# Kernel tuning notes

Hardware: AMD Instinct MI355X
Metric: run time of the kernel (lower is better)

Reference implementation:

```python
import jax, jax.numpy as jnp
import numpy as np

B, N, F, I = 4, 1024, 32, 8
DIM, DN, NF = 256, 64, 100
H, HD = 4, 64  # heads, head_dim (H*HD == DIM)
EPS = 1e-5


def setup_inputs() -> dict:
    key = jax.random.key(0)
    ks = jax.random.split(key, 24)
    def p(k, shape, s=0.05):
        return jax.random.normal(k, shape, jnp.float32) * s
    return {
        "x": jax.random.normal(ks[0], (B, N, F, I), jnp.float32),
        "idx": jax.random.randint(ks[1], (F,), 0, NF),
        "ctx": jax.random.normal(ks[2], (B, 1, DN), jnp.float32),
        "Wp": p(ks[3], (NF, DIM * I)),          # in_projection table
        "Bp": p(ks[4], (NF, DIM)),               # feature_bias table
        "q_emb": p(ks[5], (1, DIM)),             # queries table
        "cln_kv_W": p(ks[6], (DN, 2 * DIM)), "cln_kv_b": jnp.zeros((2 * DIM,), jnp.float32),
        "cln_q_W": p(ks[7], (DN, 2 * DIM)),  "cln_q_b": jnp.zeros((2 * DIM,), jnp.float32),
        "cln_h_W": p(ks[8], (DN, 2 * DIM)),  "cln_h_b": jnp.zeros((2 * DIM,), jnp.float32),
        "Wq": p(ks[9], (DIM, DIM)), "Wk": p(ks[10], (DIM, DIM)),
        "Wv": p(ks[11], (DIM, DIM)), "Wo": p(ks[12], (DIM, DIM)),
        "W1": p(ks[13], (DIM, 4 * DIM)), "b1": jnp.zeros((4 * DIM,), jnp.float32),
        "W2": p(ks[14], (4 * DIM, DIM)), "b2": jnp.zeros((DIM,), jnp.float32),
    }


def _ln(x):
    m = x.mean(-1, keepdims=True)
    v = ((x - m) ** 2).mean(-1, keepdims=True)
    return (x - m) * jax.lax.rsqrt(v + EPS)


def _cln(x, c, W, b):
    # adaptive layernorm: ln(x) * (1 + scale(ctx)) + shift(ctx)
    h = _ln(x)
    s, sh = jnp.split(c @ W + b, 2, axis=-1)
    return h * (1.0 + s) + sh


def reference(x, idx, ctx, Wp, Bp, q_emb, cln_kv_W, cln_kv_b, cln_q_W, cln_q_b,
              cln_h_W, cln_h_b, Wq, Wk, Wv, Wo, W1, b1, W2, b2):
    b_, n_, f_, i_ = x.shape
    # gather per-feature projection weights and biases
    w = Wp[idx].reshape(f_, DIM, i_)                 # [f, d, i]
    bias = Bp[idx][None]                              # [1, f, d] (broadcasts b,n)
    kv = jnp.einsum('bnfi,fdi->bnfd', x, w)           # [b, n, f, d]
    c = ctx[:, :, None, :]                            # [b, 1, 1, dn]
    kv = _cln(kv, c, cln_kv_W, cln_kv_b) + bias
    q = jnp.broadcast_to(q_emb[None, None], (b_, n_, 1, DIM))
    # cross-attention (pre-norm, conditional)
    qn = _cln(q, c, cln_q_W, cln_q_b)
    qh = (qn @ Wq).reshape(b_, n_, 1, H, HD)
    kh = (kv @ Wk).reshape(b_, n_, f_, H, HD)
    vh = (kv @ Wv).reshape(b_, n_, f_, H, HD)
    att = jnp.einsum('bnqhe,bnfhe->bnhqf', qh, kh) / np.sqrt(HD).astype(np.float32)
    att = jax.nn.softmax(att, axis=-1)
    o = jnp.einsum('bnhqf,bnfhe->bnqhe', att, vh).reshape(b_, n_, 1, DIM) @ Wo
    h = q + o
    # MLP (pre-norm, conditional)
    hn = _cln(h, c, cln_h_W, cln_h_b)
    h = h + (jax.nn.gelu(hn @ W1 + b1) @ W2 + b2)
    return h[:, :, 0, :]                              # squeeze query dim -> [b, n, d]
```

## Files before the change

kernel.cpp:

```cpp
#include <hip/hip_runtime.h>
#include <cmath>

#define EPSV 1e-5f
using f4 = float4;

typedef __attribute__((ext_vector_type(8))) short bfrag;
typedef __attribute__((ext_vector_type(4))) float ffrag;

#define WS_SKV   0
#define WS_SHKV  1024
#define WS_SH    2048
#define WS_SHH   3072
#define WS_A     4096
#define WS_R     8192
#define WS_HT    4202496
#define WS_L     5251072
#define WS_G     6299648
#define WS_GB    WS_G
#define WS_HNB   (WS_G + 2097152)
#define WS_W1T   (WS_G + 2621440)
#define WS_W2T   (WS_G + 2752512)
#define WS_MT    (WS_G + 2883584)

#define FMA8(acc, s, wa, wb) \
  acc[0]=fmaf((s),(wa).x,acc[0]); acc[1]=fmaf((s),(wa).y,acc[1]); \
  acc[2]=fmaf((s),(wa).z,acc[2]); acc[3]=fmaf((s),(wa).w,acc[3]); \
  acc[4]=fmaf((s),(wb).x,acc[4]); acc[5]=fmaf((s),(wb).y,acc[5]); \
  acc[6]=fmaf((s),(wb).z,acc[6]); acc[7]=fmaf((s),(wb).w,acc[7]);

#define DOT8(res, v, wa, wb) \
  res = fmaf((v)[0],(wa).x,res); res = fmaf((v)[1],(wa).y,res); \
  res = fmaf((v)[2],(wa).z,res); res = fmaf((v)[3],(wa).w,res); \
  res = fmaf((v)[4],(wb).x,res); res = fmaf((v)[5],(wb).y,res); \
  res = fmaf((v)[6],(wb).z,res); res = fmaf((v)[7],(wb).w,res);

__device__ __forceinline__ float bfly32(float v){
  v += __shfl_xor(v, 1);  v += __shfl_xor(v, 2);  v += __shfl_xor(v, 4);
  v += __shfl_xor(v, 8);  v += __shfl_xor(v, 16);
  return v;
}

__device__ __forceinline__ float gelu_fast(float x){
  float z2 = 1.5957691216057308f*(x + 0.044715f*x*x*x);
  return x / (1.0f + __expf(-z2));
}

__device__ __forceinline__ unsigned short f2bf(float x){
  union { float f; unsigned u; } v; v.f = x;
  unsigned r = v.u + 0x7fffu + ((v.u >> 16) & 1u);
  return (unsigned short)(r >> 16);
}
__device__ __forceinline__ void bf2x(unsigned u, float& a, float& b){
  union { unsigned u; float f; } x, y;
  x.u = u << 16; y.u = u & 0xffff0000u;
  a = x.f; b = y.f;
}

__global__ __launch_bounds__(256) void kw_conv(
  const float* __restrict__ W1, const float* __restrict__ W2,
  float* __restrict__ ws)
{
  __shared__ unsigned short lt[64][68];
  const int tid = threadIdx.x;
  int blk = blockIdx.x;
  const float* src; unsigned short* dst; int K, N, K0, N0;
  if (blk < 64){
    src = W1; dst = (unsigned short*)(ws + WS_W1T);
    K = 256; N = 1024; K0 = (blk >> 4)*64; N0 = (blk & 15)*64;
  } else {
    blk -= 64;
    src = W2; dst = (unsigned short*)(ws + WS_W2T);
    K = 1024; N = 256; K0 = (blk >> 2)*64; N0 = (blk & 3)*64;
  }
  #pragma unroll
  for (int i=0;i<4;++i){
    int r = i*16 + (tid>>4);
    int c = (tid&15)*4;
    f4 v = *(const f4*)(src + (size_t)(K0+r)*N + N0 + c);
    lt[r][c]   = f2bf(v.x); lt[r][c+1] = f2bf(v.y);
    lt[r][c+2] = f2bf(v.z); lt[r][c+3] = f2bf(v.w);
  }
  __syncthreads();
  #pragma unroll
  for (int i=0;i<4;++i){
    int n  = i*16 + (tid>>4);
    int kc = (tid&15)*4;
    ushort4 u;
    u.x = lt[kc][n]; u.y = lt[kc+1][n]; u.z = lt[kc+2][n]; u.w = lt[kc+3][n];
    *(ushort4*)(dst + (size_t)(N0+n)*K + K0 + kc) = u;
  }
}

__global__ __launch_bounds__(256) void km_conv(
  const float* __restrict__ Wv, const float* __restrict__ Wo,
  float* __restrict__ ws)
{
  __shared__ float wvs[4*64];
  __shared__ float wos[64*256];
  const int tid = threadIdx.x;
  const int h   = blockIdx.x >> 6;
  const int dg4 = blockIdx.x & 63;
  {
    int d = tid >> 6, e = tid & 63;
    wvs[d*64+e] = Wv[(size_t)(dg4*4 + d)*256 + h*64 + e];
  }
  {
    int e = tid >> 2, c = (tid & 3)*64;
    const float* src = Wo + (size_t)(h*64 + e)*256 + c;
    #pragma unroll
    for (int i=0;i<16;++i)
      *(f4*)&wos[e*256 + c + i*4] = *(const f4*)(src + i*4);
  }
  __syncthreads();
  float acc[4] = {};
  for (int e=0;e<64;++e){
    float wo = wos[e*256 + tid];
    acc[0] = fmaf(wvs[0*64+e], wo, acc[0]);
    acc[1] = fmaf(wvs[1*64+e], wo, acc[1]);
    acc[2] = fmaf(wvs[2*64+e], wo, acc[2]);
    acc[3] = fmaf(wvs[3*64+e], wo, acc[3]);
  }
  unsigned short* Mt = (unsigned short*)(ws + WS_MT);
  ushort4 u;
  u.x = f2bf(acc[0]); u.y = f2bf(acc[1]); u.z = f2bf(acc[2]); u.w = f2bf(acc[3]);
  *(ushort4*)(Mt + (size_t)tid*1024 + h*256 + dg4*4) = u;
}

__global__ __launch_bounds__(256) void k0_all(
    const float* __restrict__ ctx, const float* __restrict__ q_emb,
    const float* __restrict__ Wkv, const float* __restrict__ bkv,
    const float* __restrict__ Wqc, const float* __restrict__ bqc,
    const float* __restrict__ Whc, const float* __restrict__ bhc,
    const float* __restrict__ Wq,  const float* __restrict__ Wk,
    float* __restrict__ ws)
{
  const int b = blockIdx.x >> 2, h = blockIdx.x & 3;
  const int tid = threadIdx.x;
  __shared__ float c[64], qn[256], ph[256], qh64[64], red[8];
  if (tid < 64) c[tid] = ctx[b*64 + tid];
  __syncthreads();

  float skv = bkv[tid],      shkv = bkv[256+tid];
  float sq  = bqc[tid],      shq  = bqc[256+tid];
  float sh  = bhc[tid],      shh  = bhc[256+tid];
  #pragma unroll 8
  for (int j=0;j<64;++j){
    float cj = c[j];
    skv  = fmaf(cj, Wkv[j*512 + tid],       skv);
    shkv = fmaf(cj, Wkv[j*512 + 256 + tid], shkv);
    sq   = fmaf(cj, Wqc[j*512 + tid],       sq);
    shq  = fmaf(cj, Wqc[j*512 + 256 + tid], shq);
    sh   = fmaf(cj, Whc[j*512 + tid],       sh);
    shh  = fmaf(cj, Whc[j*512 + 256 + tid], shh);
  }
  if (h == 0){
    ws[WS_SKV  + b*256 + tid] = skv;
    ws[WS_SHKV + b*256 + tid] = shkv;
    ws[WS_SH   + b*256 + tid] = sh;
    ws[WS_SHH  + b*256 + tid] = shh;
  }

  float qe = q_emb[tid];
  float s1r = qe, s2r = qe*qe;
  for (int mm=1;mm<64;mm<<=1){ s1r += __shfl_xor(s1r,mm); s2r += __shfl_xor(s2r,mm); }
  int wv = tid>>6, ln = tid&63;
  if (ln==0){ red[wv*2]=s1r; red[wv*2+1]=s2r; }
  __syncthreads();
  float S1 = red[0]+red[2]+red[4]+red[6];
  float S2 = red[1]+red[3]+red[5]+red[7];
  float mean = S1*(1.0f/256.0f);
  float var  = S2*(1.0f/256.0f) - mean*mean;
  float rs   = rsqrtf(var + EPSV);
  qn[tid] = (qe-mean)*rs*(1.0f+sq) + shq;
  __syncthreads();

  {
    const int t = tid & 63, ks = tid >> 6;
    float p = 0.f;
    const float* wq = Wq + (size_t)(ks*64)*256 + h*64 + t;
    #pragma unroll 8
    for (int d=0; d<64; ++d) p = fmaf(qn[ks*64+d], wq[d*256], p);
    ph[tid] = p;
  }
  __syncthreads();
  if (tid < 64) qh64[tid] = ph[tid] + ph[64+tid] + ph[128+tid] + ph[192+tid];
  __syncthreads();

  {
    float a = 0.f;
    const float* wkr = Wk + (size_t)tid*256 + h*64;
    #pragma unroll
    for (int e4=0; e4<16; ++e4){
      f4 wv4 = *(const f4*)(wkr + e4*4);
      a = fmaf(qh64[e4*4+0], wv4.x, a);
      a = fmaf(qh64[e4*4+1], wv4.y, a);
      a = fmaf(qh64[e4*4+2], wv4.z, a);
      a = fmaf(qh64[e4*4+3], wv4.w, a);
    }
    ws[WS_A + b*1024 + h*256 + tid] = 0.125f*a;
  }
}

__global__ __launch_bounds__(256,4) void k1f_attn(
  const float* __restrict__ x, const int* __restrict__ idx,
  const float* __restrict__ Wp, const float* __restrict__ Bp,
  float* __restrict__ ws)
{
  __shared__ float xs[2048];
  __shared__ float wls[4096];
  __shared__ float As[1024];

  const int tid = threadIdx.x;
  const int p0  = (blockIdx.x >> 1) * 8;
  const int half= blockIdx.x & 1;
  const int f0  = half * 16;
  const int b   = p0 >> 10;
  const int t   = tid >> 5;
  const int dg  = tid & 31;
  const int dA  = 4*dg, dB = 128 + 4*dg;

  {
    const float* xg = x + (size_t)p0*256 + tid*8;
    f4 a  = *(const f4*)xg;
    f4 bq = *(const f4*)(xg + 4);
    *(f4*)&xs[tid*8]     = a;
    *(f4*)&xs[tid*8 + 4] = bq;
  }
  *(f4*)&As[tid*4] = *(const f4*)(ws + WS_A + b*1024 + tid*4);

  f4 skA = *(const f4*)(ws + WS_SKV  + b*256 + dA);
  f4 skB = *(const f4*)(ws + WS_SKV  + b*256 + dB);
  f4 shA = *(const f4*)(ws + WS_SHKV + b*256 + dA);
  f4 shB = *(const f4*)(ws + WS_SHKV + b*256 + dB);
  float coef[8] = {1.f+skA.x,1.f+skA.y,1.f+skA.z,1.f+skA.w,
                   1.f+skB.x,1.f+skB.y,1.f+skB.z,1.f+skB.w};
  float shk[8]  = {shA.x,shA.y,shA.z,shA.w, shB.x,shB.y,shB.z,shB.w};

  int r0 = idx[f0], r1 = idx[f0+1];
  f4 u0 = *(const f4*)(Wp + (size_t)r0*2048 + tid*8);
  f4 u1 = *(const f4*)(Wp + (size_t)r0*2048 + tid*8 + 4);
  f4 u2 = *(const f4*)(Wp + (size_t)r1*2048 + tid*8);
  f4 u3 = *(const f4*)(Wp + (size_t)r1*2048 + tid*8 + 4);

  float l[4] = {0.f,0.f,0.f,0.f};
  float racc[4][8] = {};

  for (int fi = 0; fi < 8; ++fi){
    const int f = f0 + fi*2;
    __syncthreads();
    wls[0*256+tid]=u0.x; wls[1*256+tid]=u0.y; wls[2*256+tid]=u0.z; wls[3*256+tid]=u0.w;
    wls[4*256+tid]=u1.x; wls[5*256+tid]=u1.y; wls[6*256+tid]=u1.z; wls[7*256+tid]=u1.w;
    wls[2048+0*256+tid]=u2.x; wls[2048+1*256+tid]=u2.y;
    wls[2048+2*256+tid]=u2.z; wls[2048+3*256+tid]=u2.w;
    wls[2048+4*256+tid]=u3.x; wls[2048+5*256+tid]=u3.y;
    wls[2048+6*256+tid]=u3.z; wls[2048+7*256+tid]=u3.w;
    __syncthreads();

    f4 ba0 = *(const f4*)(Bp + (size_t)r0*256 + dA);
    f4 bb0 = *(const f4*)(Bp + (size_t)r0*256 + dB);
    f4 ba1 = *(const f4*)(Bp + (size_t)r1*256 + dA);
    f4 bb1 = *(const f4*)(Bp + (size_t)r1*256 + dB);

    const int fn = (fi < 7) ? f + 2 : f0;
    int rn0 = idx[fn], rn1 = idx[fn+1];
    u0 = *(const f4*)(Wp + (size_t)rn0*2048 + tid*8);
    u1 = *(const f4*)(Wp + (size_t)rn0*2048 + tid*8 + 4);
    u2 = *(const f4*)(Wp + (size_t)rn1*2048 + tid*8);
    u3 = *(const f4*)(Wp + (size_t)rn1*2048 + tid*8 + 4);

    #pragma unroll
    for (int sub=0; sub<2; ++sub){
      const float* wrow = wls + sub*2048;
      const int fc = f + sub;
      f4 ba = sub ? ba1 : ba0;
      f4 bb = sub ? bb1 : bb0;

      f4 xa = *(const f4*)&xs[t*256 + fc*8];
      f4 xb = *(const f4*)&xs[t*256 + fc*8 + 4];
      float xf[8] = {xa.x,xa.y,xa.z,xa.w, xb.x,xb.y,xb.z,xb.w};

      float val[8] = {};
      #pragma unroll
      for (int i=0;i<8;++i){
        f4 wa  = *(const f4*)&wrow[i*256 + dA];
        f4 wbv = *(const f4*)&wrow[i*256 + dB];
        FMA8(val, xf[i], wa, wbv);
      }

      float s=0.f, ss=0.f;
      #pragma unroll
      for (int jj=0;jj<8;++jj){ s += val[jj]; ss = fmaf(val[jj],val[jj],ss); }
      s = bfly32(s); ss = bfly32(ss);
      float mean = s*(1.f/256.f);
      float var  = ss*(1.f/256.f) - mean*mean;
      float rsg  = rsqrtf(var + EPSV);
      float mrs  = mean*rsg;

      float off[8] = {shk[0]+ba.x, shk[1]+ba.y, shk[2]+ba.z, shk[3]+ba.w,
                      shk[4]+bb.x, shk[5]+bb.y, shk[6]+bb.z, shk[7]+bb.w};
      float kvl[8];
      #pragma unroll
      for (int jj=0;jj<8;++jj)
        kvl[jj] = fmaf(fmaf(val[jj], rsg, -mrs), coef[jj], off[jj]);

      #pragma unroll
      for (int h=0;h<4;++h){
        f4 Aa = *(const f4*)&As[h*256 + dA];
        f4 Ab = *(const f4*)&As[h*256 + dB];
        float lg = 0.f;
        DOT8(lg, kvl, Aa, Ab);
        lg = bfly32(lg);
        float pp = __expf(lg);
        l[h] += pp;
        #pragma unroll
        for (int jj=0;jj<8;++jj)
          racc[h][jj] = fmaf(pp, kvl[jj], racc[h][jj]);
      }
    }
    r0 = rn0; r1 = rn1;
  }

  unsigned short* Pr = (unsigned short*)(ws + WS_R);
  size_t base = (size_t)(half*4096 + p0 + t) * 1024;
  #pragma unroll
  for (int h=0;h<4;++h){
    ushort4 ua, ub;
    ua.x=f2bf(racc[h][0]); ua.y=f2bf(racc[h][1]); ua.z=f2bf(racc[h][2]); ua.w=f2bf(racc[h][3]);
    ub.x=f2bf(racc[h][4]); ub.y=f2bf(racc[h][5]); ub.z=f2bf(racc[h][6]); ub.w=f2bf(racc[h][7]);
    *(ushort4*)(Pr + base + h*256 + dA) = ua;
    *(ushort4*)(Pr + base + h*256 + dB) = ub;
  }
  if (dg == 0){
    float* Lp = ws + WS_L;
    #pragma unroll
    for (int h=0;h<4;++h) Lp[(size_t)(half*4096 + p0 + t)*4 + h] = l[h];
  }
}

__global__ __launch_bounds__(256) void kc_comb(float* __restrict__ ws)
{
  unsigned short* Pr = (unsigned short*)(ws + WS_R);
  const float* Lp = ws + WS_L;
  const int tid = threadIdx.x;
  const int p0 = blockIdx.x * 8;
  #pragma unroll
  for (int k=0;k<4;++k){
    size_t e0 = (size_t)p0*1024 + (size_t)k*2048 + (size_t)tid*8;
    int t = (int)(e0 >> 10);
    int h = (int)((e0 >> 8) & 3);
    float inv = 1.f / (Lp[(size_t)t*4 + h] + Lp[(size_t)(4096 + t)*4 + h]);
    uint4 a  = *(const uint4*)(Pr + e0);
    uint4 bq = *(const uint4*)(Pr + 4194304 + e0);
    unsigned au[4] = {a.x, a.y, a.z, a.w};
    unsigned bu[4] = {bq.x, bq.y, bq.z, bq.w};
    unsigned r[4];
    #pragma unroll
    for (int i=0;i<4;++i){
      float alo, ahi, blo, bhi;
      bf2x(au[i], alo, ahi);
      bf2x(bu[i], blo, bhi);
      float lo = (alo + blo) * inv;
      float hi = (ahi + bhi) * inv;
      r[i] = ((unsigned)f2bf(hi) << 16) | (unsigned)f2bf(lo);
    }
    *(uint4*)(Pr + e0) = make_uint4(r[0], r[1], r[2], r[3]);
  }
}

__global__ __launch_bounds__(256) void k2g_mfma(float* __restrict__ ws)
{
  __shared__ unsigned short aT[2][32*40];
  __shared__ unsigned short bT[2][64*40];
  const unsigned short* rb = (const unsigned short*)(ws + WS_R);
  const unsigned short* mt = (const unsigned short*)(ws + WS_MT);

  const int tid = threadIdx.x;
  const int M0 = (blockIdx.x >> 2) * 32;
  const int N0 = (blockIdx.x & 3) * 64;
  const int lane = tid & 63;
  const int wid = tid >> 6;
  const int wm = wid >> 1, wn = wid & 1;
  const int m16 = lane & 15, q = lane >> 4;

  const int sa_m = tid >> 3, sa_k = (tid & 7) * 4;
  const int sb_n = tid >> 2, sb_k = (tid & 3) * 8;

  ushort4 ua;
  f4 ub;
  ua = *(const ushort4*)(rb + (size_t)(M0 + sa_m)*1024 + sa_k);
  ub = *(const f4*)(mt + (size_t)(N0 + sb_n)*1024 + sb_k);

  ffrag acc[2];
  acc[0] = (ffrag){0.f,0.f,0.f,0.f};
  acc[1] = (ffrag){0.f,0.f,0.f,0.f};

  for (int ks=0; ks<32; ++ks){
    const int buf = ks & 1;
    *(ushort4*)&aT[buf][sa_m*40 + sa_k] = ua;
    *(f4*)&bT[buf][sb_n*40 + sb_k]      = ub;
    __syncthreads();
    int kn = (ks < 31) ? ks+1 : 31;
    ua = *(const ushort4*)(rb + (size_t)(M0 + sa_m)*1024 + kn*32 + sa_k);
    ub = *(const f4*)(mt + (size_t)(N0 + sb_n)*1024 + kn*32 + sb_k);

    bfrag af, bf0, bf1;
    af  = *(const bfrag*)&aT[buf][(wm*16 + m16)*40 + q*8];
    bf0 = *(const bfrag*)&bT[buf][(wn*32 + m16)*40 + q*8];
    bf1 = *(const bfrag*)&bT[buf][(wn*32 + 16 + m16)*40 + q*8];
    acc[0] = __builtin_amdgcn_mfma_f32_16x16x32_bf16(bf0, af, acc[0], 0, 0, 0);
    acc[1] = __builtin_amdgcn_mfma_f32_16x16x32_bf16(bf1, af, acc[1], 0, 0, 0);
  }

  const int m = M0 + wm*16 + m16;
  #pragma unroll
  for (int j=0;j<2;++j){
    const int n4 = N0 + wn*32 + j*16 + q*4;
    *(f4*)(ws + WS_HT + (size_t)m*256 + n4) =
      make_float4(acc[j][0], acc[j][1], acc[j][2], acc[j][3]);
  }
}

__global__ __launch_bounds__(256) void ke_ln(
  const float* __restrict__ q_emb, float* __restrict__ ws)
{
  const int tid = threadIdx.x;
  const int p0 = blockIdx.x * 8;
  const int b  = p0 >> 10;
  const int tq = tid >> 5, jq = tid & 31;
  const int cA = 4*jq, cB = 128 + 4*jq;

  float* op = ws + WS_HT + (size_t)(p0+tq)*256;
  f4 oA = *(const f4*)(op + cA);
  f4 oB = *(const f4*)(op + cB);
  f4 qA = *(const f4*)(q_emb + cA);
  f4 qB = *(const f4*)(q_emb + cB);
  float ht[8] = {oA.x+qA.x, oA.y+qA.y, oA.z+qA.z, oA.w+qA.w,
                 oB.x+qB.x, oB.y+qB.y, oB.z+qB.z, oB.w+qB.w};
  float s=0.f, ss=0.f;
  #pragma unroll
  for (int jj=0;jj<8;++jj){ s += ht[jj]; ss = fmaf(ht[jj],ht[jj],ss); }
  s = bfly32(s); ss = bfly32(ss);
  float mean = s*(1.f/256.f);
  float var  = ss*(1.f/256.f) - mean*mean;
  float rsg  = rsqrtf(var + EPSV);
  f4 sH0 = *(const f4*)(ws + WS_SH  + b*256 + cA);
  f4 sH1 = *(const f4*)(ws + WS_SH  + b*256 + cB);
  f4 hH0 = *(const f4*)(ws + WS_SHH + b*256 + cA);
  f4 hH1 = *(const f4*)(ws + WS_SHH + b*256 + cB);
  float sHv[8]  = {sH0.x,sH0.y,sH0.z,sH0.w, sH1.x,sH1.y,sH1.z,sH1.w};
  float hHv[8]  = {hH0.x,hH0.y,hH0.z,hH0.w, hH1.x,hH1.y,hH1.z,hH1.w};
  float hnv[8];
  #pragma unroll
  for (int jj=0;jj<8;++jj)
    hnv[jj] = (ht[jj]-mean)*rsg*(1.f+sHv[jj]) + hHv[jj];

  *(f4*)(op+cA) = make_float4(ht[0],ht[1],ht[2],ht[3]);
  *(f4*)(op+cB) = make_float4(ht[4],ht[5],ht[6],ht[7]);
  unsigned short* hnb = (unsigned short*)(ws + WS_HNB);
  ushort4 uA, uB;
  uA.x=f2bf(hnv[0]); uA.y=f2bf(hnv[1]); uA.z=f2bf(hnv[2]); uA.w=f2bf(hnv[3]);
  uB.x=f2bf(hnv[4]); uB.y=f2bf(hnv[5]); uB.z=f2bf(hnv[6]); uB.w=f2bf(hnv[7]);
  *(ushort4*)(hnb + (size_t)(p0+tq)*256 + cA) = uA;
  *(ushort4*)(hnb + (size_t)(p0+tq)*256 + cB) = uB;
}

__global__ __launch_bounds__(256) void k3_mfma(
  const float* __restrict__ b1, float* __restrict__ ws)
{
  __shared__ unsigned short aT[2][64*40];
  __shared__ unsigned short bT[2][128*40];
  const unsigned short* hnb = (const unsigned short*)(ws + WS_HNB);
  const unsigned short* w1t = (const unsigned short*)(ws + WS_W1T);
  unsigned short* gb = (unsigned short*)(ws + WS_GB);

  const int tid = threadIdx.x;
  const int M0 = (blockIdx.x >> 3) * 64;
  const int N0 = (blockIdx.x & 7) * 128;
  const int lane = tid & 63;
  const int wid = tid >> 6;
  const int wm = wid >> 1, wn = wid & 1;
  const int m16 = lane & 15, q = lane >> 4;

  const int sa_m = tid >> 2, sa_k = (tid & 3) * 8;
  const int sb_n = tid >> 1, sb_k = (tid & 1) * 16;

  f4 ua, ub0, ub1;
  ua  = *(const f4*)(hnb + (size_t)(M0 + sa_m)*256 + sa_k);
  ub0 = *(const f4*)(w1t + (size_t)(N0 + sb_n)*256 + sb_k);
  ub1 = *(const f4*)(w1t + (size_t)(N0 + sb_n)*256 + sb_k + 8);

  ffrag acc[2][4];
  #pragma unroll
  for (int i=0;i<2;++i)
    #pragma unroll
    for (int j=0;j<4;++j) acc[i][j] = (ffrag){0.f,0.f,0.f,0.f};

  for (int ks=0; ks<8; ++ks){
    const int buf = ks & 1;
    *(f4*)&aT[buf][sa_m*40 + sa_k]     = ua;
    *(f4*)&bT[buf][sb_n*40 + sb_k]     = ub0;
    *(f4*)&bT[buf][sb_n*40 + sb_k + 8] = ub1;
    __syncthreads();
    int kn = (ks < 7) ? ks+1 : 7;
    ua  = *(const f4*)(hnb + (size_t)(M0 + sa_m)*256 + kn*32 + sa_k);
    ub0 = *(const f4*)(w1t + (size_t)(N0 + sb_n)*256 + kn*32 + sb_k);
    ub1 = *(const f4*)(w1t + (size_t)(N0 + sb_n)*256 + kn*32 + sb_k + 8);

    bfrag af[2], bf_[4];
    af[0] = *(const bfrag*)&aT[buf][(wm*32 + m16)*40 + q*8];
    af[1] = *(const bfrag*)&aT[buf][(wm*32 + 16 + m16)*40 + q*8];
    #pragma unroll
    for (int j=0;j<4;++j)
      bf_[j] = *(const bfrag*)&bT[buf][(wn*64 + j*16 + m16)*40 + q*8];
    #pragma unroll
    for (int i=0;i<2;++i)
      #pragma unroll
      for (int j=0;j<4;++j)
        acc[i][j] = __builtin_amdgcn_mfma_f32_16x16x32_bf16(bf_[j], af[i], acc[i][j], 0, 0, 0);
  }

  #pragma unroll
  for (int i=0;i<2;++i){
    const int m = M0 + wm*32 + i*16 + m16;
    #pragma unroll
    for (int j=0;j<4;++j){
      const int n4 = N0 + wn*64 + j*16 + q*4;
      f4 bv = *(const f4*)(b1 + n4);
      ushort4 u;
      u.x = f2bf(gelu_fast(acc[i][j][0] + bv.x));
      u.y = f2bf(gelu_fast(acc[i][j][1] + bv.y));
      u.z = f2bf(gelu_fast(acc[i][j][2] + bv.z));
      u.w = f2bf(gelu_fast(acc[i][j][3] + bv.w));
      *(ushort4*)(gb + (size_t)m*1024 + n4) = u;
    }
  }
}

__global__ __launch_bounds__(256) void k4_mfma(
  const float* __restrict__ b2, const float* __restrict__ ws_c,
  float* __restrict__ ws, float* __restrict__ out)
{
  __shared__ unsigned short aT[2][32*40];
  __shared__ unsigned short bT[2][64*40];
  const unsigned short* gb  = (const unsigned short*)(ws_c + WS_GB);
  const unsigned short* w2t = (const unsigned short*)(ws_c + WS_W2T);

  const int tid = threadIdx.x;
  const int M0 = (blockIdx.x >> 2) * 32;
  const int N0 = (blockIdx.x & 3) * 64;
  const int lane = tid & 63;
  const int wid = tid >> 6;
  const int wm = wid >> 1, wn = wid & 1;
  const int m16 = lane & 15, q = lane >> 4;

  const int sa_m = tid >> 3, sa_k = (tid & 7) * 4;
  const int sb_n = tid >> 2, sb_k = (tid & 3) * 8;

  ushort4 ua;
  f4 ub;
  ua = *(const ushort4*)(gb  + (size_t)(M0 + sa_m)*1024 + sa_k);
  ub = *(const f4*)(w2t + (size_t)(N0 + sb_n)*1024 + sb_k);

  ffrag acc[2];
  acc[0] = (ffrag){0.f,0.f,0.f,0.f};
  acc[1] = (ffrag){0.f,0.f,0.f,0.f};

  for (int ks=0; ks<32; ++ks){
    const int buf = ks & 1;
    *(ushort4*)&aT[buf][sa_m*40 + sa_k] = ua;
    *(f4*)&bT[buf][sb_n*40 + sb_k]      = ub;
    __syncthreads();
    int kn = (ks < 31) ? ks+1 : 31;
    ua = *(const ushort4*)(gb  + (size_t)(M0 + sa_m)*1024 + kn*32 + sa_k);
    ub = *(const f4*)(w2t + (size_t)(N0 + sb_n)*1024 + kn*32 + sb_k);

    bfrag af, bf0, bf1;
    af  = *(const bfrag*)&aT[buf][(wm*16 + m16)*40 + q*8];
    bf0 = *(const bfrag*)&bT[buf][(wn*32 + m16)*40 + q*8];
    bf1 = *(const bfrag*)&bT[buf][(wn*32 + 16 + m16)*40 + q*8];
    acc[0] = __builtin_amdgcn_mfma_f32_16x16x32_bf16(bf0, af, acc[0], 0, 0, 0);
    acc[1] = __builtin_amdgcn_mfma_f32_16x16x32_bf16(bf1, af, acc[1], 0, 0, 0);
  }

  const int m = M0 + wm*16 + m16;
  #pragma unroll
  for (int j=0;j<2;++j){
    const int n4 = N0 + wn*32 + j*16 + q*4;
    f4 bv = *(const f4*)(b2 + n4);
    f4 hv = *(const f4*)(ws + WS_HT + (size_t)m*256 + n4);
    *(f4*)(out + (size_t)m*256 + n4) =
      make_float4(acc[j][0]+bv.x+hv.x, acc[j][1]+bv.y+hv.y,
                  acc[j][2]+bv.z+hv.z, acc[j][3]+bv.w+hv.w);
  }
}

extern "C" void kernel_launch(void* const* d_in, const int* in_sizes, int n_in,
                              void* d_out, int out_size, void* d_ws, size_t ws_size,
                              hipStream_t stream)
{
  const float* x    = (const float*)d_in[0];
  const int*   idx  = (const int*)  d_in[1];
  const float* ctx  = (const float*)d_in[2];
  const float* Wp   = (const float*)d_in[3];
  const float* Bp   = (const float*)d_in[4];
  const float* qemb = (const float*)d_in[5];
  const float* Wkv  = (const float*)d_in[6];
  const float* bkv  = (const float*)d_in[7];
  const float* Wqc  = (const float*)d_in[8];
  const float* bqc  = (const float*)d_in[9];
  const float* Whc  = (const float*)d_in[10];
  const float* bhc  = (const float*)d_in[11];
  const float* Wq   = (const float*)d_in[12];
  const float* Wk   = (const float*)d_in[13];
  const float* Wv   = (const float*)d_in[14];
  const float* Wo   = (const float*)d_in[15];
  const float* W1   = (const float*)d_in[16];
  const float* b1   = (const float*)d_in[17];
  const float* W2   = (const float*)d_in[18];
  const float* b2   = (const float*)d_in[19];
  float* ws  = (float*)d_ws;
  float* out = (float*)d_out;

  hipLaunchKernelGGL(kw_conv,  dim3(128),  dim3(256), 0, stream, W1, W2, ws);
  hipLaunchKernelGGL(km_conv,  dim3(256),  dim3(256), 0, stream, Wv, Wo, ws);
  hipLaunchKernelGGL(k0_all,   dim3(16),   dim3(256), 0, stream,
                     ctx, qemb, Wkv, bkv, Wqc, bqc, Whc, bhc, Wq, Wk, ws);
  hipLaunchKernelGGL(k1f_attn, dim3(1024), dim3(256), 0, stream, x, idx, Wp, Bp, ws);
  hipLaunchKernelGGL(kc_comb,  dim3(512),  dim3(256), 0, stream, ws);
  hipLaunchKernelGGL(k2g_mfma, dim3(512),  dim3(256), 0, stream, ws);
  hipLaunchKernelGGL(ke_ln,    dim3(512),  dim3(256), 0, stream, qemb, ws);
  hipLaunchKernelGGL(k3_mfma,  dim3(512),  dim3(256), 0, stream, b1, ws);
  hipLaunchKernelGGL(k4_mfma,  dim3(512),  dim3(256), 0, stream, b2, ws, ws, out);
}
```

Before: 202.7 us.

## Fuse split-softmax combine into GEMM, merge weight-convert kernels, use DPP reductions

The separate kernel that combined the two feature-half partial attention outputs is removed. Its normalization by the summed softmax denominators now happens inside the MFMA GEMM's A-tile staging, which loads both partial buffers and scales them on the fly. This removes one launch and a full read-modify-write pass over the partial outputs. The two weight-conversion kernels are merged into one launch. In the attention kernel the per-head query vectors move from shared memory to registers, and the 32-lane butterfly shuffles become DPP row ops plus one shuffle. In exchange, the GEMM reads twice the A data per tile and does extra conversion work, and the attention kernel holds more registers.

```diff
diff --git a/kernel.cpp b/kernel.cpp
--- a/kernel.cpp
+++ b/kernel.cpp
@@ -40,6 +40,21 @@
   return v;
 }
 
+template<int CTRL>
+__device__ __forceinline__ float dpp_add(float v){
+  int x = __builtin_bit_cast(int, v);
+  int y = __builtin_amdgcn_update_dpp(0, x, CTRL, 0xf, 0xf, true);
+  return v + __builtin_bit_cast(float, y);
+}
+__device__ __forceinline__ float red32(float v){
+  v = dpp_add<0xB1>(v);
+  v = dpp_add<0x4E>(v);
+  v = dpp_add<0x124>(v);
+  v = dpp_add<0x128>(v);
+  v += __shfl_xor(v, 16);
+  return v;
+}
+
 __device__ __forceinline__ float gelu_fast(float x){
   float z2 = 1.5957691216057308f*(x + 0.044715f*x*x*x);
   return x / (1.0f + __expf(-z2));
@@ -50,80 +65,84 @@
   unsigned r = v.u + 0x7fffu + ((v.u >> 16) & 1u);
   return (unsigned short)(r >> 16);
 }
-__device__ __forceinline__ void bf2x(unsigned u, float& a, float& b){
-  union { unsigned u; float f; } x, y;
-  x.u = u << 16; y.u = u & 0xffff0000u;
-  a = x.f; b = y.f;
-}
-
-__global__ __launch_bounds__(256) void kw_conv(
+__device__ __forceinline__ float bfu(unsigned short u){
+  union { unsigned u; float f; } v; v.u = ((unsigned)u) << 16; return v.f;
+}
+__device__ __forceinline__ ushort4 comb4(ushort4 a, ushort4 b, float inv){
+  ushort4 r;
+  r.x = f2bf((bfu(a.x)+bfu(b.x))*inv);
+  r.y = f2bf((bfu(a.y)+bfu(b.y))*inv);
+  r.z = f2bf((bfu(a.z)+bfu(b.z))*inv);
+  r.w = f2bf((bfu(a.w)+bfu(b.w))*inv);
+  return r;
+}
+
+__global__ __launch_bounds__(256) void kwm_conv(
   const float* __restrict__ W1, const float* __restrict__ W2,
+  const float* __restrict__ Wv, const float* __restrict__ Wo,
   float* __restrict__ ws)
 {
-  __shared__ unsigned short lt[64][68];
   const int tid = threadIdx.x;
   int blk = blockIdx.x;
-  const float* src; unsigned short* dst; int K, N, K0, N0;
-  if (blk < 64){
-    src = W1; dst = (unsigned short*)(ws + WS_W1T);
-    K = 256; N = 1024; K0 = (blk >> 4)*64; N0 = (blk & 15)*64;
+  if (blk < 128){
+    __shared__ unsigned short lt[64][68];
+    const float* src; unsigned short* dst; int K, N, K0, N0;
+    if (blk < 64){
+      src = W1; dst = (unsigned short*)(ws + WS_W1T);
+      K = 256; N = 1024; K0 = (blk >> 4)*64; N0 = (blk & 15)*64;
+    } else {
+      blk -= 64;
+      src = W2; dst = (unsigned short*)(ws + WS_W2T);
+      K = 1024; N = 256; K0 = (blk >> 2)*64; N0 = (blk & 3)*64;
+    }
+    #pragma unroll
+    for (int i=0;i<4;++i){
+      int r = i*16 + (tid>>4);
+      int c = (tid&15)*4;
+      f4 v = *(const f4*)(src + (size_t)(K0+r)*N + N0 + c);
+      lt[r][c]   = f2bf(v.x); lt[r][c+1] = f2bf(v.y);
+      lt[r][c+2] = f2bf(v.z); lt[r][c+3] = f2bf(v.w);
+    }
+    __syncthreads();
+    #pragma unroll
+    for (int i=0;i<4;++i){
+      int n  = i*16 + (tid>>4);
+      int kc = (tid&15)*4;
+      ushort4 u;
+      u.x = lt[kc][n]; u.y = lt[kc+1][n]; u.z = lt[kc+2][n]; u.w = lt[kc+3][n];
+      *(ushort4*)(dst + (size_t)(N0+n)*K + K0 + kc) = u;
+    }
   } else {
-    blk -= 64;
-    src = W2; dst = (unsigned short*)(ws + WS_W2T);
-    K = 1024; N = 256; K0 = (blk >> 2)*64; N0 = (blk & 3)*64;
-  }
-  #pragma unroll
-  for (int i=0;i<4;++i){
-    int r = i*16 + (tid>>4);
-    int c = (tid&15)*4;
-    f4 v = *(const f4*)(src + (size_t)(K0+r)*N + N0 + c);
-    lt[r][c]   = f2bf(v.x); lt[r][c+1] = f2bf(v.y);
-    lt[r][c+2] = f2bf(v.z); lt[r][c+3] = f2bf(v.w);
-  }
-  __syncthreads();
-  #pragma unroll
-  for (int i=0;i<4;++i){
-    int n  = i*16 + (tid>>4);
-    int kc = (tid&15)*4;
+    blk -= 128;
+    __shared__ float wvs[4*64];
+    __shared__ float wos[64*256];
+    const int h   = blk >> 6;
+    const int dg4 = blk & 63;
+    {
+      int d = tid >> 6, e = tid & 63;
+      wvs[d*64+e] = Wv[(size_t)(dg4*4 + d)*256 + h*64 + e];
+    }
+    {
+      int e = tid >> 2, c = (tid & 3)*64;
+      const float* src = Wo + (size_t)(h*64 + e)*256 + c;
+      #pragma unroll
+      for (int i=0;i<16;++i)
+        *(f4*)&wos[e*256 + c + i*4] = *(const f4*)(src + i*4);
+    }
+    __syncthreads();
+    float acc[4] = {};
+    for (int e=0;e<64;++e){
+      float wo = wos[e*256 + tid];
+      acc[0] = fmaf(wvs[0*64+e], wo, acc[0]);
+      acc[1] = fmaf(wvs[1*64+e], wo, acc[1]);
+      acc[2] = fmaf(wvs[2*64+e], wo, acc[2]);
+      acc[3] = fmaf(wvs[3*64+e], wo, acc[3]);
+    }
+    unsigned short* Mt = (unsigned short*)(ws + WS_MT);
     ushort4 u;
-    u.x = lt[kc][n]; u.y = lt[kc+1][n]; u.z = lt[kc+2][n]; u.w = lt[kc+3][n];
-    *(ushort4*)(dst + (size_t)(N0+n)*K + K0 + kc) = u;
-  }
-}
-
-__global__ __launch_bounds__(256) void km_conv(
-  const float* __restrict__ Wv, const float* __restrict__ Wo,
-  float* __restrict__ ws)
-{
-  __shared__ float wvs[4*64];
-  __shared__ float wos[64*256];
-  const int tid = threadIdx.x;
-  const int h   = blockIdx.x >> 6;
-  const int dg4 = blockIdx.x & 63;
-  {
-    int d = tid >> 6, e = tid & 63;
-    wvs[d*64+e] = Wv[(size_t)(dg4*4 + d)*256 + h*64 + e];
-  }
-  {
-    int e = tid >> 2, c = (tid & 3)*64;
-    const float* src = Wo + (size_t)(h*64 + e)*256 + c;
-    #pragma unroll
-    for (int i=0;i<16;++i)
-      *(f4*)&wos[e*256 + c + i*4] = *(const f4*)(src + i*4);
-  }
-  __syncthreads();
-  float acc[4] = {};
-  for (int e=0;e<64;++e){
-    float wo = wos[e*256 + tid];
-    acc[0] = fmaf(wvs[0*64+e], wo, acc[0]);
-    acc[1] = fmaf(wvs[1*64+e], wo, acc[1]);
-    acc[2] = fmaf(wvs[2*64+e], wo, acc[2]);
-    acc[3] = fmaf(wvs[3*64+e], wo, acc[3]);
-  }
-  unsigned short* Mt = (unsigned short*)(ws + WS_MT);
-  ushort4 u;
-  u.x = f2bf(acc[0]); u.y = f2bf(acc[1]); u.z = f2bf(acc[2]); u.w = f2bf(acc[3]);
-  *(ushort4*)(Mt + (size_t)tid*1024 + h*256 + dg4*4) = u;
+    u.x = f2bf(acc[0]); u.y = f2bf(acc[1]); u.z = f2bf(acc[2]); u.w = f2bf(acc[3]);
+    *(ushort4*)(Mt + (size_t)tid*1024 + h*256 + dg4*4) = u;
+  }
 }
 
 __global__ __launch_bounds__(256) void k0_all(
@@ -208,7 +227,6 @@
 {
   __shared__ float xs[2048];
   __shared__ float wls[4096];
-  __shared__ float As[1024];
 
   const int tid = threadIdx.x;
   const int p0  = (blockIdx.x >> 1) * 8;
@@ -226,7 +244,12 @@
     *(f4*)&xs[tid*8]     = a;
     *(f4*)&xs[tid*8 + 4] = bq;
   }
-  *(f4*)&As[tid*4] = *(const f4*)(ws + WS_A + b*1024 + tid*4);
+  f4 Ar[4][2];
+  #pragma unroll
+  for (int h=0;h<4;++h){
+    Ar[h][0] = *(const f4*)(ws + WS_A + b*1024 + h*256 + dA);
+    Ar[h][1] = *(const f4*)(ws + WS_A + b*1024 + h*256 + dB);
+  }
 
   f4 skA = *(const f4*)(ws + WS_SKV  + b*256 + dA);
   f4 skB = *(const f4*)(ws + WS_SKV  + b*256 + dB);
@@ -290,7 +313,7 @@
       float s=0.f, ss=0.f;
       #pragma unroll
       for (int jj=0;jj<8;++jj){ s += val[jj]; ss = fmaf(val[jj],val[jj],ss); }
-      s = bfly32(s); ss = bfly32(ss);
+      s = red32(s); ss = red32(ss);
       float mean = s*(1.f/256.f);
       float var  = ss*(1.f/256.f) - mean*mean;
       float rsg  = rsqrtf(var + EPSV);
@@ -305,11 +328,9 @@
 
       #pragma unroll
       for (int h=0;h<4;++h){
-        f4 Aa = *(const f4*)&As[h*256 + dA];
-        f4 Ab = *(const f4*)&As[h*256 + dB];
         float lg = 0.f;
-        DOT8(lg, kvl, Aa, Ab);
-        lg = bfly32(lg);
+        DOT8(lg, kvl, Ar[h][0], Ar[h][1]);
+        lg = red32(lg);
         float pp = __expf(lg);
         l[h] += pp;
         #pragma unroll
@@ -337,42 +358,15 @@
   }
 }
 
-__global__ __launch_bounds__(256) void kc_comb(float* __restrict__ ws)
-{
-  unsigned short* Pr = (unsigned short*)(ws + WS_R);
-  const float* Lp = ws + WS_L;
-  const int tid = threadIdx.x;
-  const int p0 = blockIdx.x * 8;
-  #pragma unroll
-  for (int k=0;k<4;++k){
-    size_t e0 = (size_t)p0*1024 + (size_t)k*2048 + (size_t)tid*8;
-    int t = (int)(e0 >> 10);
-    int h = (int)((e0 >> 8) & 3);
-    float inv = 1.f / (Lp[(size_t)t*4 + h] + Lp[(size_t)(4096 + t)*4 + h]);
-    uint4 a  = *(const uint4*)(Pr + e0);
-    uint4 bq = *(const uint4*)(Pr + 4194304 + e0);
-    unsigned au[4] = {a.x, a.y, a.z, a.w};
-    unsigned bu[4] = {bq.x, bq.y, bq.z, bq.w};
-    unsigned r[4];
-    #pragma unroll
-    for (int i=0;i<4;++i){
-      float alo, ahi, blo, bhi;
-      bf2x(au[i], alo, ahi);
-      bf2x(bu[i], blo, bhi);
-      float lo = (alo + blo) * inv;
-      float hi = (ahi + bhi) * inv;
-      r[i] = ((unsigned)f2bf(hi) << 16) | (unsigned)f2bf(lo);
-    }
-    *(uint4*)(Pr + e0) = make_uint4(r[0], r[1], r[2], r[3]);
-  }
-}
-
 __global__ __launch_bounds__(256) void k2g_mfma(float* __restrict__ ws)
 {
   __shared__ unsigned short aT[2][32*40];
   __shared__ unsigned short bT[2][64*40];
-  const unsigned short* rb = (const unsigned short*)(ws + WS_R);
+  __shared__ float invs[128];
+  const unsigned short* P0 = (const unsigned short*)(ws + WS_R);
+  const unsigned short* P1 = P0 + 4194304;
   const unsigned short* mt = (const unsigned short*)(ws + WS_MT);
+  const float* Lp = ws + WS_L;
 
   const int tid = threadIdx.x;
   const int M0 = (blockIdx.x >> 2) * 32;
@@ -385,10 +379,16 @@
   const int sa_m = tid >> 3, sa_k = (tid & 7) * 4;
   const int sb_n = tid >> 2, sb_k = (tid & 3) * 8;
 
-  ushort4 ua;
-  f4 ub;
-  ua = *(const ushort4*)(rb + (size_t)(M0 + sa_m)*1024 + sa_k);
-  ub = *(const f4*)(mt + (size_t)(N0 + sb_n)*1024 + sb_k);
+  if (tid < 128){
+    int lt = tid >> 2, h = tid & 3;
+    invs[tid] = 1.f / (Lp[(size_t)(M0 + lt)*4 + h] +
+                       Lp[(size_t)(4096 + M0 + lt)*4 + h]);
+  }
+
+  ushort4 ua0 = *(const ushort4*)(P0 + (size_t)(M0 + sa_m)*1024 + sa_k);
+  ushort4 ua1 = *(const ushort4*)(P1 + (size_t)(M0 + sa_m)*1024 + sa_k);
+  f4 ub = *(const f4*)(mt + (size_t)(N0 + sb_n)*1024 + sb_k);
+  __syncthreads();
 
   ffrag acc[2];
   acc[0] = (ffrag){0.f,0.f,0.f,0.f};
@@ -396,12 +396,14 @@
 
   for (int ks=0; ks<32; ++ks){
     const int buf = ks & 1;
-    *(ushort4*)&aT[buf][sa_m*40 + sa_k] = ua;
+    float inv = invs[sa_m*4 + (ks >> 3)];
+    *(ushort4*)&aT[buf][sa_m*40 + sa_k] = comb4(ua0, ua1, inv);
     *(f4*)&bT[buf][sb_n*40 + sb_k]      = ub;
     __syncthreads();
     int kn = (ks < 31) ? ks+1 : 31;
-    ua = *(const ushort4*)(rb + (size_t)(M0 + sa_m)*1024 + kn*32 + sa_k);
-    ub = *(const f4*)(mt + (size_t)(N0 + sb_n)*1024 + kn*32 + sb_k);
+    ua0 = *(const ushort4*)(P0 + (size_t)(M0 + sa_m)*1024 + kn*32 + sa_k);
+    ua1 = *(const ushort4*)(P1 + (size_t)(M0 + sa_m)*1024 + kn*32 + sa_k);
+    ub  = *(const f4*)(mt + (size_t)(N0 + sb_n)*1024 + kn*32 + sb_k);
 
     bfrag af, bf0, bf1;
     af  = *(const bfrag*)&aT[buf][(wm*16 + m16)*40 + q*8];
@@ -621,12 +623,10 @@
   float* ws  = (float*)d_ws;
   float* out = (float*)d_out;
 
-  hipLaunchKernelGGL(kw_conv,  dim3(128),  dim3(256), 0, stream, W1, W2, ws);
-  hipLaunchKernelGGL(km_conv,  dim3(256),  dim3(256), 0, stream, Wv, Wo, ws);
+  hipLaunchKernelGGL(kwm_conv, dim3(384),  dim3(256), 0, stream, W1, W2, Wv, Wo, ws);
   hipLaunchKernelGGL(k0_all,   dim3(16),   dim3(256), 0, stream,
                      ctx, qemb, Wkv, bkv, Wqc, bqc, Whc, bhc, Wq, Wk, ws);
   hipLaunchKernelGGL(k1f_attn, dim3(1024), dim3(256), 0, stream, x, idx, Wp, Bp, ws);
-  hipLaunchKernelGGL(kc_comb,  dim3(512),  dim3(256), 0, stream, ws);
   hipLaunchKernelGGL(k2g_mfma, dim3(512),  dim3(256), 0, stream, ws);
   hipLaunchKernelGGL(ke_ln,    dim3(512),  dim3(256), 0, stream, qemb, ws);
   hipLaunchKernelGGL(k3_mfma,  dim3(512),  dim3(256), 0, stream, b1, ws);
```

Result: faster. 193.8 us (-4.4%).
